# Optimization experiments

Hardware: AMD Instinct MI355X
Metric: run time of the kernel (lower is better)

## Reference

```python
import jax, jax.numpy as jnp
import numpy as np

BETA = 0.25  # commitment loss weight


def setup_inputs() -> dict:
    key = jax.random.key(0)
    k1, k2 = jax.random.split(key)
    z = jax.random.normal(k1, (16, 256, 64, 64), dtype=jnp.float32)      # encoder latent, NCHW
    codebook = jax.random.normal(k2, (1024, 256), dtype=jnp.float32)     # [n_e, e_dim]
    return {"z": z, "codebook": codebook}


def reference(z, codebook):
    B, C, H, W = z.shape
    z_bhwc = jnp.transpose(z, (0, 2, 3, 1))            # [B,H,W,C]
    zf = z_bhwc.reshape(-1, C)                          # [N,C], N = B*H*W
    # squared L2 distance to every codeword: ||z||^2 + ||e||^2 - 2 z.e
    d = ((zf * zf).sum(axis=1, keepdims=True)
         + (codebook * codebook).sum(axis=1)[None, :]
         - 2.0 * zf @ codebook.T)                       # [N, n_e]
    idx = jnp.argmin(d, axis=1)                         # [N] nearest codeword
    zq = codebook[idx].reshape(B, H, W, C)              # irregular gather
    # VQ loss: codebook term + beta * commitment term
    loss = (BETA * jnp.mean((jax.lax.stop_gradient(zq) - z_bhwc) ** 2)
            + jnp.mean((zq - jax.lax.stop_gradient(z_bhwc)) ** 2))
    # straight-through estimator
    zq_st = z_bhwc + jax.lax.stop_gradient(zq - z_bhwc)
    return jnp.transpose(zq_st, (0, 3, 1, 2)), loss
```

## Files before the change

### kernel.cpp

```cpp
#include <hip/hip_runtime.h>
#include <cfloat>

#define C_DIM 256
#define HW    4096
#define NE    1024
#define NPIX  65536
#define TAU   0.15f
#define ZSTR  264

typedef __attribute__((ext_vector_type(8))) _Float16 half8_t;
typedef __attribute__((ext_vector_type(4))) float floatx4;

__device__ __forceinline__ unsigned int fenc(float f) {
  unsigned int u = __float_as_uint(f);
  return (u & 0x80000000u) ? ~u : (u | 0x80000000u);
}


__global__ __launch_bounds__(256)
void e2_kernel(const float* __restrict__ cb, float* __restrict__ e2) {
  const int wave = (blockIdx.x * 256 + (int)threadIdx.x) >> 6;
  const int lane = threadIdx.x & 63;
  const float4 v = *(const float4*)(cb + (size_t)wave * C_DIM + lane * 4);
  float s = v.x * v.x + v.y * v.y + v.z * v.z + v.w * v.w;
  #pragma unroll
  for (int off = 32; off; off >>= 1) s += __shfl_down(s, off, 64);
  if (lane == 0) e2[wave] = s;
}

__global__ __launch_bounds__(256)
void pack_kernel(const float* __restrict__ cb, _Float16* __restrict__ EhfP) {
  const int g = blockIdx.x >> 3, it = blockIdx.x & 7;
  const int sidx = it * 256 + (int)threadIdx.x;
  const int ks = sidx >> 8, i = (sidx >> 6) & 3, lane = sidx & 63;
  const int ln = lane & 15, quad = lane >> 4;
  const float* src = cb + (size_t)(g * 64 + i * 16 + ln) * C_DIM + ks * 32 + quad * 8;
  const float4 v0 = *(const float4*)(src);
  const float4 v1 = *(const float4*)(src + 4);
  half8_t h;
  h[0] = (_Float16)v0.x; h[1] = (_Float16)v0.y; h[2] = (_Float16)v0.z; h[3] = (_Float16)v0.w;
  h[4] = (_Float16)v1.x; h[5] = (_Float16)v1.y; h[6] = (_Float16)v1.z; h[7] = (_Float16)v1.w;
  *(half8_t*)(EhfP + (size_t)g * 16384 + (size_t)sidx * 8) = h;
}

__global__ __launch_bounds__(256, 2)
void screen_kernel(const float* __restrict__ z, const _Float16* __restrict__ EhfP,
                   const float* __restrict__ e2, int* __restrict__ idx_out,
                   unsigned char* __restrict__ flags, unsigned long long* __restrict__ key64,
                   int* __restrict__ clist, int* __restrict__ ccount) {
  __shared__ __align__(16) _Float16 Zl[128 * ZSTR];
  __shared__ float e2l[NE];

  const int tid = threadIdx.x;
  const int ptile = blockIdx.x * 128;
  const int b = ptile >> 12, pb = ptile & 4095;
  const float* zb = z + (size_t)b * (C_DIM * HW) + pb;

  #pragma unroll
  for (int it = 0; it < 16; ++it) {
    const int flat = it * 256 + tid;
    const int p = flat & 127, kb = flat >> 7;
    float f[8];
    #pragma unroll
    for (int j = 0; j < 8; ++j) f[j] = zb[(size_t)(kb * 8 + j) * HW + p];
    half8_t h;
    #pragma unroll
    for (int j = 0; j < 8; ++j) h[j] = (_Float16)f[j];
    *(half8_t*)&Zl[p * ZSTR + kb * 8] = h;
  }
  #pragma unroll
  for (int i = 0; i < 4; ++i) e2l[i * 256 + tid] = e2[i * 256 + tid];
  __syncthreads();

  const int lane = tid & 63;
  const int w = tid >> 6;
  const int wc = w & 1, wp = w >> 1;
  const int ln = lane & 15, quad = lane >> 4;

  const _Float16* aBase = EhfP + (size_t)wc * 16384 + (size_t)lane * 8;
  const char* rowB[4];
  #pragma unroll
  for (int j = 0; j < 4; ++j)
    rowB[j] = (const char*)(&Zl[(wp * 64 + j * 16 + ln) * ZSTR + quad * 8]);

  float d1[4], d2[4]; int i1[4];
  #pragma unroll
  for (int j = 0; j < 4; ++j) { d1[j] = FLT_MAX; d2[j] = FLT_MAX; i1[j] = 0; }

  half8_t abuf[2][4], bbuf[2][4];
  #pragma unroll
  for (int i = 0; i < 4; ++i) abuf[0][i] = *(const half8_t*)(aBase + i * 512);
  #pragma unroll
  for (int j = 0; j < 4; ++j) bbuf[0][j] = *(const half8_t*)(rowB[j]);

  for (int nc = 0; nc < 8; ++nc) {
    floatx4 acc[4][4];
    #pragma unroll
    for (int i = 0; i < 4; ++i)
      #pragma unroll
      for (int j = 0; j < 4; ++j) acc[i][j] = (floatx4){0.f, 0.f, 0.f, 0.f};

    #pragma unroll
    for (int ks = 0; ks < 8; ++ks) {
      const int cur = ks & 1, nxt = cur ^ 1;
      const int s1 = nc * 8 + ks + 1;
      const int sp = s1 > 63 ? 63 : s1;
      const size_t aoff = (size_t)(sp >> 3) * 32768 + (size_t)(sp & 7) * 2048;
      const int bks = sp & 7;
      #pragma unroll
      for (int i = 0; i < 4; ++i) abuf[nxt][i] = *(const half8_t*)(aBase + aoff + i * 512);
      #pragma unroll
      for (int j = 0; j < 4; ++j) bbuf[nxt][j] = *(const half8_t*)(rowB[j] + bks * 64);
      #pragma unroll
      for (int i = 0; i < 4; ++i)
        #pragma unroll
        for (int j = 0; j < 4; ++j)
          acc[i][j] = __builtin_amdgcn_mfma_f32_16x16x32_f16(abuf[cur][i], bbuf[cur][j], acc[i][j], 0, 0, 0);
    }

    const int cwb = nc * 128 + wc * 64;
    #pragma unroll
    for (int i = 0; i < 4; ++i) {
      const int cw0 = cwb + i * 16 + quad * 4;
      float ee[4];
      #pragma unroll
      for (int r = 0; r < 4; ++r) ee[r] = e2l[cw0 + r];
      #pragma unroll
      for (int j = 0; j < 4; ++j) {
        #pragma unroll
        for (int r = 0; r < 4; ++r) {
          const float d = fmaf(-2.0f, acc[i][j][r], ee[r]);
          const bool lt = d < d1[j];
          const float hi = lt ? d1[j] : d;
          d1[j] = lt ? d : d1[j];
          i1[j] = lt ? (cw0 + r) : i1[j];
          d2[j] = fminf(d2[j], hi);
        }
      }
    }
  }

  #pragma unroll
  for (int j = 0; j < 4; ++j) {
    #pragma unroll
    for (int m = 16; m <= 32; m <<= 1) {
      const float od1 = __shfl_xor(d1[j], m, 64);
      const int   oi1 = __shfl_xor(i1[j], m, 64);
      const float od2 = __shfl_xor(d2[j], m, 64);
      const bool take = (od1 < d1[j]) || (od1 == d1[j] && oi1 < i1[j]);
      const float hi = take ? d1[j] : od1;
      d1[j] = take ? od1 : d1[j];
      i1[j] = take ? oi1 : i1[j];
      d2[j] = fminf(fminf(d2[j], od2), hi);
    }
  }

  __syncthreads();
  float* rd1 = (float*)Zl;
  int*   ri1 = (int*)Zl + 256;
  float* rd2 = (float*)Zl + 512;
  if (lane < 16) {
    #pragma unroll
    for (int j = 0; j < 4; ++j) {
      const int p = wp * 64 + j * 16 + ln;
      rd1[wc * 128 + p] = d1[j];
      ri1[wc * 128 + p] = i1[j];
      rd2[wc * 128 + p] = d2[j];
    }
  }
  __syncthreads();
  if (tid < 128) {
    const float a1 = rd1[tid], b1 = rd1[128 + tid];
    const int   ai = ri1[tid], bi = ri1[128 + tid];
    const float a2 = rd2[tid], b2 = rd2[128 + tid];
    const bool take = (b1 < a1) || (b1 == a1 && bi < ai);
    const float d1f = take ? b1 : a1;
    const int   i1f = take ? bi : ai;
    const float hi  = take ? a1 : b1;
    const float d2f = fminf(fminf(a2, b2), hi);
    const int gp = ptile + tid;
    idx_out[gp] = i1f;
    const bool contested = (d2f - d1f) <= TAU;
    flags[gp] = contested ? 1 : 0;
    if (contested) {
      key64[gp] = ~0ULL;
      const int pos = atomicAdd(ccount, 1);
      clist[pos] = gp;
    }
  }
}

__global__ __launch_bounds__(256)
void rescan_kernel(const float* __restrict__ z, const float* __restrict__ cb,
                   const float* __restrict__ e2, const int* __restrict__ clist,
                   const int* __restrict__ ccount,
                   unsigned long long* __restrict__ key64) {
  __shared__ __align__(16) float zl[256 * 8];
  __shared__ int pxs[8];
  __shared__ unsigned long long bestk[8];
  const int n = *ccount;
  const int ngroups = (n + 7) >> 3;
  const int nunits = ngroups * 8;
  for (int u = blockIdx.x; u < nunits; u += gridDim.x) {
    const int g = u >> 3, oct = u & 7;
    const int base = g * 8;
    const int npx = min(8, n - base);
    if ((int)threadIdx.x < 8) {
      pxs[threadIdx.x] = clist[base + min((int)threadIdx.x, npx - 1)];
      bestk[threadIdx.x] = ~0ULL;
    }
    __syncthreads();
    {
      const int k = threadIdx.x;
      float tmp[8];
      #pragma unroll
      for (int i = 0; i < 8; ++i) {
        const int gp = pxs[i];
        tmp[i] = z[(size_t)(gp >> 12) * (C_DIM * HW) + (size_t)k * HW + (gp & 4095)];
      }
      #pragma unroll
      for (int i = 0; i < 8; ++i) zl[k * 8 + i] = tmp[i];
    }
    __syncthreads();
    const int cw = oct * 128 + ((int)threadIdx.x & 127);
    const int ph = (int)threadIdx.x >> 7;
    const float* row = cb + (size_t)cw * C_DIM;
    float dot[4] = {0.f, 0.f, 0.f, 0.f};
    for (int k0 = 0; k0 < 256; k0 += 4) {
      const float4 ev = *(const float4*)(row + k0);
      const float e4[4] = {ev.x, ev.y, ev.z, ev.w};
      #pragma unroll
      for (int kk = 0; kk < 4; ++kk) {
        const float4 zz = *(const float4*)&zl[(k0 + kk) * 8 + ph * 4];
        dot[0] = fmaf(e4[kk], zz.x, dot[0]);
        dot[1] = fmaf(e4[kk], zz.y, dot[1]);
        dot[2] = fmaf(e4[kk], zz.z, dot[2]);
        dot[3] = fmaf(e4[kk], zz.w, dot[3]);
      }
    }
    const float ee = e2[cw];
    #pragma unroll
    for (int i = 0; i < 4; ++i) {
      const float d = fmaf(-2.0f, dot[i], ee);
      const unsigned long long key = ((unsigned long long)fenc(d) << 32) | (unsigned)cw;
      atomicMin(&bestk[ph * 4 + i], key);
    }
    __syncthreads();
    if ((int)threadIdx.x < npx) atomicMin(&key64[pxs[threadIdx.x]], bestk[threadIdx.x]);
    __syncthreads();
  }
}

__global__ __launch_bounds__(256)
void gather_loss_kernel(const float* __restrict__ z, const float* __restrict__ cb,
                        const int* __restrict__ idx, const unsigned char* __restrict__ flags,
                        const unsigned long long* __restrict__ key64,
                        float* __restrict__ out, float* __restrict__ acc) {
  const int pg = blockIdx.x * 256 + threadIdx.x;
  int id = idx[pg];
  if (flags[pg]) id = (int)(unsigned)(key64[pg] & 0xFFFFFFFFull);
  const int b = pg >> 12, p = pg & 4095;
  const float* zrow = z   + (size_t)b * (C_DIM * HW) + p;
  float*       orow = out + (size_t)b * (C_DIM * HW) + p;
  const float* erow = cb + (size_t)id * C_DIM;
  float s = 0.f;
  for (int c0 = 0; c0 < C_DIM; c0 += 4) {
    const float4 ev = *(const float4*)(erow + c0);
    const float e[4] = {ev.x, ev.y, ev.z, ev.w};
    #pragma unroll
    for (int j = 0; j < 4; ++j) {
      const float zv = zrow[(size_t)(c0 + j) * HW];
      const float dd = e[j] - zv;
      s = fmaf(dd, dd, s);
      orow[(size_t)(c0 + j) * HW] = e[j];
    }
  }
  __shared__ float sdata[256];
  sdata[threadIdx.x] = s;
  __syncthreads();
  #pragma unroll
  for (int off = 128; off; off >>= 1) {
    if (threadIdx.x < (unsigned)off) sdata[threadIdx.x] += sdata[threadIdx.x + off];
    __syncthreads();
  }
  if (threadIdx.x == 0) atomicAdd(acc, sdata[0]);
}

__global__ void finalize_kernel(const float* __restrict__ acc, float* __restrict__ loss_out) {
  *loss_out = 1.25f * (*acc) * (1.0f / 16777216.0f);
}

extern "C" void kernel_launch(void* const* d_in, const int* in_sizes, int n_in,
                              void* d_out, int out_size, void* d_ws, size_t ws_size,
                              hipStream_t stream) {
  const float* z  = (const float*)d_in[0];
  const float* cb = (const float*)d_in[1];
  float* out = (float*)d_out;
  char* ws = (char*)d_ws;

  float*              acc    = (float*)ws;
  int*                ccount = (int*)(ws + 8);
  float*              e2     = (float*)(ws + 4096);
  _Float16*           EhfP   = (_Float16*)(ws + 8192);
  int*                idx    = (int*)(ws + 532480);
  unsigned char*      flags  = (unsigned char*)(ws + 794624);
  unsigned long long* key64  = (unsigned long long*)(ws + 860160);
  int*                clist  = (int*)(ws + 1384448);

  (void)hipMemsetAsync(d_ws, 0, 16, stream);
  e2_kernel<<<NE / 4, 256, 0, stream>>>(cb, e2);
  pack_kernel<<<128, 256, 0, stream>>>(cb, EhfP);
  screen_kernel<<<NPIX / 128, 256, 0, stream>>>(z, EhfP, e2, idx, flags, key64, clist, ccount);
  rescan_kernel<<<1024, 256, 0, stream>>>(z, cb, e2, clist, ccount, key64);
  gather_loss_kernel<<<NPIX / 256, 256, 0, stream>>>(z, cb, idx, flags, key64, out, acc);
  finalize_kernel<<<1, 1, 0, stream>>>(acc, out + 16777216);
}
```

Before: 238.7 us.

## Rescan whole codebook per contested pixel and drop flags/key64 indirection

The rescan kernel now gives each block 4 contested pixels and scans all 1024 codewords per pixel. It reduces with wave shuffles and one LDS atomic per wave, then writes the final index straight into idx. This replaces the old 8-pixel by 8-octant split that used global 64-bit atomicMin, and it removes the flags and key64 arrays along with their writes and reads in screen and gather. The screen kernel also deepens A-operand prefetch to two steps ahead with a 4-slot buffer, which uses more registers and may hurt occupancy at the launch bound of 2.

Measured after the change: 228.9 us. 1.04x faster.

```diff
diff --git a/kernel.cpp b/kernel.cpp
--- a/kernel.cpp
+++ b/kernel.cpp
@@ -46,7 +46,6 @@
 __global__ __launch_bounds__(256, 2)
 void screen_kernel(const float* __restrict__ z, const _Float16* __restrict__ EhfP,
                    const float* __restrict__ e2, int* __restrict__ idx_out,
-                   unsigned char* __restrict__ flags, unsigned long long* __restrict__ key64,
                    int* __restrict__ clist, int* __restrict__ ccount) {
   __shared__ __align__(16) _Float16 Zl[128 * ZSTR];
   __shared__ float e2l[NE];
@@ -87,9 +86,11 @@
   #pragma unroll
   for (int j = 0; j < 4; ++j) { d1[j] = FLT_MAX; d2[j] = FLT_MAX; i1[j] = 0; }
 
-  half8_t abuf[2][4], bbuf[2][4];
+  half8_t abuf[4][4], bbuf[2][4];
   #pragma unroll
   for (int i = 0; i < 4; ++i) abuf[0][i] = *(const half8_t*)(aBase + i * 512);
+  #pragma unroll
+  for (int i = 0; i < 4; ++i) abuf[1][i] = *(const half8_t*)(aBase + 2048 + i * 512);
   #pragma unroll
   for (int j = 0; j < 4; ++j) bbuf[0][j] = *(const half8_t*)(rowB[j]);
 
@@ -102,20 +103,28 @@
 
     #pragma unroll
     for (int ks = 0; ks < 8; ++ks) {
-      const int cur = ks & 1, nxt = cur ^ 1;
-      const int s1 = nc * 8 + ks + 1;
-      const int sp = s1 > 63 ? 63 : s1;
-      const size_t aoff = (size_t)(sp >> 3) * 32768 + (size_t)(sp & 7) * 2048;
-      const int bks = sp & 7;
-      #pragma unroll
-      for (int i = 0; i < 4; ++i) abuf[nxt][i] = *(const half8_t*)(aBase + aoff + i * 512);
-      #pragma unroll
-      for (int j = 0; j < 4; ++j) bbuf[nxt][j] = *(const half8_t*)(rowB[j] + bks * 64);
+      const int s = nc * 8 + ks;
+      const int ca = ks & 3;
+      const int pa = (ks + 2) & 3;
+      const int cbs = ks & 1;
+      const int pbs = cbs ^ 1;
+      {
+        const int sp = s + 2 > 63 ? 63 : s + 2;
+        const size_t aoff = (size_t)(sp >> 3) * 32768 + (size_t)(sp & 7) * 2048;
+        #pragma unroll
+        for (int i = 0; i < 4; ++i) abuf[pa][i] = *(const half8_t*)(aBase + aoff + i * 512);
+      }
+      {
+        const int s1 = s + 1 > 63 ? 63 : s + 1;
+        const int bks = s1 & 7;
+        #pragma unroll
+        for (int j = 0; j < 4; ++j) bbuf[pbs][j] = *(const half8_t*)(rowB[j] + bks * 64);
+      }
       #pragma unroll
       for (int i = 0; i < 4; ++i)
         #pragma unroll
         for (int j = 0; j < 4; ++j)
-          acc[i][j] = __builtin_amdgcn_mfma_f32_16x16x32_f16(abuf[cur][i], bbuf[cur][j], acc[i][j], 0, 0, 0);
+          acc[i][j] = __builtin_amdgcn_mfma_f32_16x16x32_f16(abuf[ca][i], bbuf[cbs][j], acc[i][j], 0, 0, 0);
     }
 
     const int cwb = nc * 128 + wc * 64;
@@ -180,10 +189,7 @@
     const float d2f = fminf(fminf(a2, b2), hi);
     const int gp = ptile + tid;
     idx_out[gp] = i1f;
-    const bool contested = (d2f - d1f) <= TAU;
-    flags[gp] = contested ? 1 : 0;
-    if (contested) {
-      key64[gp] = ~0ULL;
+    if ((d2f - d1f) <= TAU) {
       const int pos = atomicAdd(ccount, 1);
       clist[pos] = gp;
     }
@@ -193,72 +199,77 @@
 __global__ __launch_bounds__(256)
 void rescan_kernel(const float* __restrict__ z, const float* __restrict__ cb,
                    const float* __restrict__ e2, const int* __restrict__ clist,
-                   const int* __restrict__ ccount,
-                   unsigned long long* __restrict__ key64) {
-  __shared__ __align__(16) float zl[256 * 8];
-  __shared__ int pxs[8];
-  __shared__ unsigned long long bestk[8];
+                   const int* __restrict__ ccount, int* __restrict__ idx_out) {
+  __shared__ __align__(16) float zl[4][C_DIM];
+  __shared__ int pxs[4];
+  __shared__ unsigned long long bestk[4];
   const int n = *ccount;
-  const int ngroups = (n + 7) >> 3;
-  const int nunits = ngroups * 8;
-  for (int u = blockIdx.x; u < nunits; u += gridDim.x) {
-    const int g = u >> 3, oct = u & 7;
-    const int base = g * 8;
-    const int npx = min(8, n - base);
-    if ((int)threadIdx.x < 8) {
-      pxs[threadIdx.x] = clist[base + min((int)threadIdx.x, npx - 1)];
+  const int ngroups = (n + 3) >> 2;
+  for (int g = blockIdx.x; g < ngroups; g += gridDim.x) {
+    const int base = g * 4;
+    if ((int)threadIdx.x < 4) {
+      pxs[threadIdx.x] = clist[min(base + (int)threadIdx.x, n - 1)];
       bestk[threadIdx.x] = ~0ULL;
     }
     __syncthreads();
     {
       const int k = threadIdx.x;
-      float tmp[8];
-      #pragma unroll
-      for (int i = 0; i < 8; ++i) {
+      #pragma unroll
+      for (int i = 0; i < 4; ++i) {
         const int gp = pxs[i];
-        tmp[i] = z[(size_t)(gp >> 12) * (C_DIM * HW) + (size_t)k * HW + (gp & 4095)];
-      }
-      #pragma unroll
-      for (int i = 0; i < 8; ++i) zl[k * 8 + i] = tmp[i];
-    }
-    __syncthreads();
-    const int cw = oct * 128 + ((int)threadIdx.x & 127);
-    const int ph = (int)threadIdx.x >> 7;
-    const float* row = cb + (size_t)cw * C_DIM;
-    float dot[4] = {0.f, 0.f, 0.f, 0.f};
-    for (int k0 = 0; k0 < 256; k0 += 4) {
-      const float4 ev = *(const float4*)(row + k0);
-      const float e4[4] = {ev.x, ev.y, ev.z, ev.w};
-      #pragma unroll
-      for (int kk = 0; kk < 4; ++kk) {
-        const float4 zz = *(const float4*)&zl[(k0 + kk) * 8 + ph * 4];
-        dot[0] = fmaf(e4[kk], zz.x, dot[0]);
-        dot[1] = fmaf(e4[kk], zz.y, dot[1]);
-        dot[2] = fmaf(e4[kk], zz.z, dot[2]);
-        dot[3] = fmaf(e4[kk], zz.w, dot[3]);
-      }
-    }
-    const float ee = e2[cw];
+        zl[i][k] = z[(size_t)(gp >> 12) * (C_DIM * HW) + (size_t)k * HW + (gp & 4095)];
+      }
+    }
+    __syncthreads();
+    unsigned long long mykey[4] = {~0ULL, ~0ULL, ~0ULL, ~0ULL};
+    #pragma unroll 1
+    for (int o = 0; o < 4; ++o) {
+      const int cw = o * 256 + (int)threadIdx.x;
+      const float* row = cb + (size_t)cw * C_DIM;
+      float dot[4] = {0.f, 0.f, 0.f, 0.f};
+      #pragma unroll 4
+      for (int k0 = 0; k0 < C_DIM; k0 += 4) {
+        const float4 ev = *(const float4*)(row + k0);
+        #pragma unroll
+        for (int i = 0; i < 4; ++i) {
+          const float4 zz = *(const float4*)&zl[i][k0];
+          dot[i] = fmaf(ev.x, zz.x, dot[i]);
+          dot[i] = fmaf(ev.y, zz.y, dot[i]);
+          dot[i] = fmaf(ev.z, zz.z, dot[i]);
+          dot[i] = fmaf(ev.w, zz.w, dot[i]);
+        }
+      }
+      const float ee = e2[cw];
+      #pragma unroll
+      for (int i = 0; i < 4; ++i) {
+        const float d = fmaf(-2.0f, dot[i], ee);
+        const unsigned long long key = ((unsigned long long)fenc(d) << 32) | (unsigned)cw;
+        mykey[i] = key < mykey[i] ? key : mykey[i];
+      }
+    }
     #pragma unroll
     for (int i = 0; i < 4; ++i) {
-      const float d = fmaf(-2.0f, dot[i], ee);
-      const unsigned long long key = ((unsigned long long)fenc(d) << 32) | (unsigned)cw;
-      atomicMin(&bestk[ph * 4 + i], key);
-    }
-    __syncthreads();
-    if ((int)threadIdx.x < npx) atomicMin(&key64[pxs[threadIdx.x]], bestk[threadIdx.x]);
+      unsigned long long k = mykey[i];
+      #pragma unroll
+      for (int off = 32; off; off >>= 1) {
+        const unsigned long long ok = __shfl_xor(k, off, 64);
+        k = ok < k ? ok : k;
+      }
+      if ((threadIdx.x & 63) == 0) atomicMin(&bestk[i], k);
+    }
+    __syncthreads();
+    if ((int)threadIdx.x < 4)
+      idx_out[pxs[threadIdx.x]] = (int)(unsigned)(bestk[threadIdx.x] & 0xFFFFFFFFull);
     __syncthreads();
   }
 }
 
 __global__ __launch_bounds__(256)
 void gather_loss_kernel(const float* __restrict__ z, const float* __restrict__ cb,
-                        const int* __restrict__ idx, const unsigned char* __restrict__ flags,
-                        const unsigned long long* __restrict__ key64,
+                        const int* __restrict__ idx,
                         float* __restrict__ out, float* __restrict__ acc) {
   const int pg = blockIdx.x * 256 + threadIdx.x;
-  int id = idx[pg];
-  if (flags[pg]) id = (int)(unsigned)(key64[pg] & 0xFFFFFFFFull);
+  const int id = idx[pg];
   const int b = pg >> 12, p = pg & 4095;
   const float* zrow = z   + (size_t)b * (C_DIM * HW) + p;
   float*       orow = out + (size_t)b * (C_DIM * HW) + p;
@@ -298,20 +309,18 @@
   float* out = (float*)d_out;
   char* ws = (char*)d_ws;
 
-  float*              acc    = (float*)ws;
-  int*                ccount = (int*)(ws + 8);
-  float*              e2     = (float*)(ws + 4096);
-  _Float16*           EhfP   = (_Float16*)(ws + 8192);
-  int*                idx    = (int*)(ws + 532480);
-  unsigned char*      flags  = (unsigned char*)(ws + 794624);
-  unsigned long long* key64  = (unsigned long long*)(ws + 860160);
-  int*                clist  = (int*)(ws + 1384448);
+  float*    acc    = (float*)ws;
+  int*      ccount = (int*)(ws + 8);
+  float*    e2     = (float*)(ws + 4096);
+  _Float16* EhfP   = (_Float16*)(ws + 8192);
+  int*      idx    = (int*)(ws + 532480);
+  int*      clist  = (int*)(ws + 794624);
 
   (void)hipMemsetAsync(d_ws, 0, 16, stream);
   e2_kernel<<<NE / 4, 256, 0, stream>>>(cb, e2);
   pack_kernel<<<128, 256, 0, stream>>>(cb, EhfP);
-  screen_kernel<<<NPIX / 128, 256, 0, stream>>>(z, EhfP, e2, idx, flags, key64, clist, ccount);
-  rescan_kernel<<<1024, 256, 0, stream>>>(z, cb, e2, clist, ccount, key64);
-  gather_loss_kernel<<<NPIX / 256, 256, 0, stream>>>(z, cb, idx, flags, key64, out, acc);
+  screen_kernel<<<NPIX / 128, 256, 0, stream>>>(z, EhfP, e2, idx, clist, ccount);
+  rescan_kernel<<<1024, 256, 0, stream>>>(z, cb, e2, clist, ccount, idx);
+  gather_loss_kernel<<<NPIX / 256, 256, 0, stream>>>(z, cb, idx, out, acc);
   finalize_kernel<<<1, 1, 0, stream>>>(acc, out + 16777216);
 }
```
